# Optimization experiments

Measured on AMD Instinct MI355X. Metric: run time of the kernel, lower is better.

The kernel has to match this reference:

```python
import jax, jax.numpy as jnp
import numpy as np

RRELU_SLOPE = (1.0 / 8.0 + 1.0 / 3.0) / 2.0  # RReLU eval-mode negative slope


def _layer(h, edge_feats, src, dst, W, b, Lw, Lb, n_nodes):
    # per-edge message: concat(src node feat, edge feat) -> linear
    msg = jnp.concatenate([h[src], edge_feats], axis=-1) @ W + b  # [E, H]
    # mean-aggregate messages by destination node (0 for isolated nodes, DGL semantics)
    s = jax.ops.segment_sum(msg, dst, num_segments=n_nodes)  # [N, H]
    cnt = jax.ops.segment_sum(jnp.ones((dst.shape[0], 1), msg.dtype), dst,
                              num_segments=n_nodes)  # [N, 1]
    agg = jnp.where(cnt > 0, s / jnp.maximum(cnt, 1.0), 0.0)
    # self-loop linear add
    agg = agg + h @ Lw + Lb
    # RReLU (eval mode = leaky relu with slope (lower+upper)/2); dropout p=0 is identity
    return jnp.where(agg >= 0, agg, agg * RRELU_SLOPE)


def setup_inputs() -> dict:
    key = jax.random.key(0)
    ks = jax.random.split(key, 12)
    N, E, D, H = 50000, 640000, 128, 128
    sc_in = 1.0 / np.sqrt(2 * D)
    sc_d = 1.0 / np.sqrt(D)
    sc_o = 1.0 / np.sqrt(2 * H)
    return {
        "node_feats": jax.random.normal(ks[0], (N, D), jnp.float32),
        "edge_feats": jax.random.normal(ks[1], (E, D), jnp.float32),
        "src": jax.random.randint(ks[2], (E,), 0, N),
        "dst": jax.random.randint(ks[3], (E,), 0, N),
        "W1": jax.random.uniform(ks[4], (2 * D, H), jnp.float32, -sc_in, sc_in),
        "b1": jnp.zeros((H,), jnp.float32),
        "L1": jax.random.uniform(ks[5], (D, H), jnp.float32, -sc_d, sc_d),
        "lb1": jnp.zeros((H,), jnp.float32),
        "W2": jax.random.uniform(ks[6], (2 * H, H), jnp.float32, -sc_in, sc_in),
        "b2": jnp.zeros((H,), jnp.float32),
        "L2": jax.random.uniform(ks[7], (H, H), jnp.float32, -sc_d, sc_d),
        "lb2": jnp.zeros((H,), jnp.float32),
        "Wo": jax.random.uniform(ks[8], (2 * H, H), jnp.float32, -sc_o, sc_o),
        "bo": jnp.zeros((H,), jnp.float32),
    }


def reference(node_feats, edge_feats, src, dst, W1, b1, L1, lb1, W2, b2, L2, lb2, Wo, bo):
    n = node_feats.shape[0]
    h1 = _layer(node_feats, edge_feats, src, dst, W1, b1, L1, lb1, n)
    h2 = _layer(h1, edge_feats, src, dst, W2, b2, L2, lb2, n)
    multihop = jnp.concatenate([h1, h2], axis=-1)  # [N, 2H]
    return multihop @ Wo + bo
```

## Files before the change

### kernel.cpp

```cpp
#include <hip/hip_runtime.h>
#include <hip/hip_bf16.h>

typedef unsigned short u16;
typedef unsigned int   u32;

using bf16x8 = __attribute__((ext_vector_type(8))) __bf16;
using f32x4  = __attribute__((ext_vector_type(4))) float;

#define SLOPE 0.22916666666666666f
#define CAP 64

static __device__ __forceinline__ u16 f2bf(float f) {
    u32 u = __float_as_uint(f);
    u += 0x7fffu + ((u >> 16) & 1u);
    return (u16)(u >> 16);
}
static __device__ __forceinline__ float bf2f(u16 h) {
    return __uint_as_float(((u32)h) << 16);
}

static __device__ __forceinline__ void gload_lds16(const u16* g, u16* l) {
    __builtin_amdgcn_global_load_lds(
        (const __attribute__((address_space(1))) void*)g,
        (__attribute__((address_space(3))) void*)l,
        16, 0, 0);
}

__global__ void k_prep(const int* __restrict__ src, const int* __restrict__ dst,
                       int* __restrict__ deg, int2* __restrict__ se,
                       const float* __restrict__ node, u16* __restrict__ nfb,
                       const float* __restrict__ W1, const float* __restrict__ L1,
                       const float* __restrict__ W2, const float* __restrict__ L2,
                       const float* __restrict__ Wo, u16* __restrict__ T,
                       int E, int n8, int gE, int gF) {
    int b = blockIdx.x, t = threadIdx.x;
    if (b < gE) {
        int i = b * 256 + t;
        if (i < E) {
            int d = dst[i];
            int p = atomicAdd(&deg[d], 1);
            if (p < CAP) se[(size_t)d * CAP + p] = make_int2(src[i], i);
        }
    } else if (b < gE + gF) {
        int i = (b - gE) * 256 + t;
        if (i < n8) {
            const float4* p = (const float4*)node + (size_t)i * 2;
            float4 a = p[0], c = p[1];
            union { u16 u[8]; uint4 v; } pk;
            pk.u[0] = f2bf(a.x); pk.u[1] = f2bf(a.y); pk.u[2] = f2bf(a.z); pk.u[3] = f2bf(a.w);
            pk.u[4] = f2bf(c.x); pk.u[5] = f2bf(c.y); pk.u[6] = f2bf(c.z); pk.u[7] = f2bf(c.w);
            *((uint4*)nfb + i) = pk.v;
        }
    } else {
        int m = b - gE - gF;
        const float* S; int rowoff;
        switch (m) {
            case 0: S = W1; rowoff = 0;   break;
            case 1: S = W1; rowoff = 128; break;
            case 2: S = L1; rowoff = 0;   break;
            case 3: S = W2; rowoff = 0;   break;
            case 4: S = W2; rowoff = 128; break;
            case 5: S = L2; rowoff = 0;   break;
            case 6: S = Wo; rowoff = 0;   break;
            default: S = Wo; rowoff = 128; break;
        }
        u16* O = T + m * 16384;
        for (int i = t; i < 16384; i += 256) {
            int c = i >> 7, k = i & 127;
            O[i] = f2bf(S[(rowoff + k) * 128 + c]);
        }
    }
}

__global__ void k_aggf(const float* __restrict__ ef, const u16* __restrict__ nfb,
                       const int2* __restrict__ se, const int* __restrict__ deg,
                       u16* __restrict__ EF, u16* __restrict__ A, int N) {
    int w = (blockIdx.x * blockDim.x + threadIdx.x) >> 6;
    int lane = threadIdx.x & 63;
    if (w >= N) return;
    int half = lane >> 5, q = lane & 31;
    int d = deg[w];
    int dc = d < CAP ? d : CAP;
    const int2* sp = se + (size_t)w * CAP;
    float e0 = 0.f, e1 = 0.f, e2 = 0.f, e3 = 0.f;
    float n0 = 0.f, n1 = 0.f, n2 = 0.f, n3 = 0.f;
    int i = 0;
    for (; i + 4 <= dc; i += 4) {
        int2 ia = sp[i + half], ib = sp[i + 2 + half];
        float4 xa = *(const float4*)(ef + (size_t)ia.y * 128 + q * 4);
        uint2  ya = *(const uint2*)(nfb + (size_t)ia.x * 128 + q * 4);
        float4 xb = *(const float4*)(ef + (size_t)ib.y * 128 + q * 4);
        uint2  yb = *(const uint2*)(nfb + (size_t)ib.x * 128 + q * 4);
        e0 += xa.x + xb.x; e1 += xa.y + xb.y; e2 += xa.z + xb.z; e3 += xa.w + xb.w;
        n0 += bf2f((u16)ya.x) + bf2f((u16)yb.x);
        n1 += bf2f((u16)(ya.x >> 16)) + bf2f((u16)(yb.x >> 16));
        n2 += bf2f((u16)ya.y) + bf2f((u16)yb.y);
        n3 += bf2f((u16)(ya.y >> 16)) + bf2f((u16)(yb.y >> 16));
    }
    for (; i + 2 <= dc; i += 2) {
        int2 ia = sp[i + half];
        float4 xa = *(const float4*)(ef + (size_t)ia.y * 128 + q * 4);
        uint2  ya = *(const uint2*)(nfb + (size_t)ia.x * 128 + q * 4);
        e0 += xa.x; e1 += xa.y; e2 += xa.z; e3 += xa.w;
        n0 += bf2f((u16)ya.x); n1 += bf2f((u16)(ya.x >> 16));
        n2 += bf2f((u16)ya.y); n3 += bf2f((u16)(ya.y >> 16));
    }
    if (i + half < dc) {
        int2 ia = sp[i + half];
        float4 xa = *(const float4*)(ef + (size_t)ia.y * 128 + q * 4);
        uint2  ya = *(const uint2*)(nfb + (size_t)ia.x * 128 + q * 4);
        e0 += xa.x; e1 += xa.y; e2 += xa.z; e3 += xa.w;
        n0 += bf2f((u16)ya.x); n1 += bf2f((u16)(ya.x >> 16));
        n2 += bf2f((u16)ya.y); n3 += bf2f((u16)(ya.y >> 16));
    }
    e0 += __shfl_xor(e0, 32); e1 += __shfl_xor(e1, 32);
    e2 += __shfl_xor(e2, 32); e3 += __shfl_xor(e3, 32);
    n0 += __shfl_xor(n0, 32); n1 += __shfl_xor(n1, 32);
    n2 += __shfl_xor(n2, 32); n3 += __shfl_xor(n3, 32);
    float sc = d > 0 ? 1.0f / (float)d : 0.0f;
    union { u16 u[4]; uint2 v; } pk;
    if (half == 0) {
        pk.u[0] = f2bf(e0 * sc); pk.u[1] = f2bf(e1 * sc);
        pk.u[2] = f2bf(e2 * sc); pk.u[3] = f2bf(e3 * sc);
        *(uint2*)(EF + (size_t)w * 128 + q * 4) = pk.v;
    } else {
        pk.u[0] = f2bf(n0 * sc); pk.u[1] = f2bf(n1 * sc);
        pk.u[2] = f2bf(n2 * sc); pk.u[3] = f2bf(n3 * sc);
        *(uint2*)(A + (size_t)w * 128 + q * 4) = pk.v;
    }
}

static __device__ __forceinline__ void add8(float* a, uint4 u) {
    a[0] += bf2f((u16)u.x); a[1] += bf2f((u16)(u.x >> 16));
    a[2] += bf2f((u16)u.y); a[3] += bf2f((u16)(u.y >> 16));
    a[4] += bf2f((u16)u.z); a[5] += bf2f((u16)(u.z >> 16));
    a[6] += bf2f((u16)u.w); a[7] += bf2f((u16)(u.w >> 16));
}

__global__ void k_aggb(const u16* __restrict__ h, const int2* __restrict__ se,
                       const int* __restrict__ deg, u16* __restrict__ out, int N) {
    int w = (blockIdx.x * blockDim.x + threadIdx.x) >> 6;
    int lane = threadIdx.x & 63;
    if (w >= N) return;
    int quarter = lane >> 4, q = lane & 15;
    int d = deg[w];
    int dc = d < CAP ? d : CAP;
    const int2* sp = se + (size_t)w * CAP;
    float a[8] = {0.f, 0.f, 0.f, 0.f, 0.f, 0.f, 0.f, 0.f};
    int i = 0;
    for (; i + 8 <= dc; i += 8) {
        int eA = sp[i + quarter].x, eB = sp[i + 4 + quarter].x;
        uint4 uA = *(const uint4*)(h + (size_t)eA * 128 + q * 8);
        uint4 uB = *(const uint4*)(h + (size_t)eB * 128 + q * 8);
        add8(a, uA); add8(a, uB);
    }
    for (; i + 4 <= dc; i += 4) {
        int eA = sp[i + quarter].x;
        uint4 uA = *(const uint4*)(h + (size_t)eA * 128 + q * 8);
        add8(a, uA);
    }
    if (i + quarter < dc) {
        int eA = sp[i + quarter].x;
        uint4 uA = *(const uint4*)(h + (size_t)eA * 128 + q * 8);
        add8(a, uA);
    }
    #pragma unroll
    for (int j = 0; j < 8; j++) {
        a[j] += __shfl_xor(a[j], 32);
        a[j] += __shfl_xor(a[j], 16);
    }
    if (quarter == 0) {
        float sc = d > 0 ? 1.0f / (float)d : 0.0f;
        union { u16 u[8]; uint4 v; } pk;
        #pragma unroll
        for (int j = 0; j < 8; j++) pk.u[j] = f2bf(a[j] * sc);
        *(uint4*)(out + (size_t)w * 128 + q * 8) = pk.v;
    }
}

#define STAGE_X(LBUF, GPTR)                                                         \
    {                                                                               \
        _Pragma("unroll")                                                           \
        for (int i_ = 0; i_ < 4; i_++) {                                            \
            int id_ = t + i_ * 256;                                                 \
            int r_ = id_ >> 4, c16_ = id_ & 15;                                     \
            int rg_ = row0 + r_; if (rg_ >= N) rg_ = N - 1;                         \
            gload_lds16((GPTR) + (size_t)rg_ * 128 + ((c16_ ^ (r_ & 15)) << 3),     \
                        (LBUF) + id_ * 8);                                          \
        }                                                                           \
    }
#define STAGE_W(GPTR)                                                               \
    {                                                                               \
        _Pragma("unroll")                                                           \
        for (int i_ = 0; i_ < 8; i_++) {                                            \
            int id_ = t + i_ * 256;                                                 \
            int cc_ = id_ >> 4, c16_ = id_ & 15;                                    \
            gload_lds16((GPTR) + cc_ * 128 + ((c16_ ^ (cc_ & 15)) << 3),            \
                        Wl + id_ * 8);                                              \
        }                                                                           \
    }
#define COMPUTE(LBUF)                                                               \
    {                                                                               \
        _Pragma("unroll")                                                           \
        for (int ks_ = 0; ks_ < 4; ks_++) {                                         \
            bf16x8 af_[2], bf_[4];                                                  \
            _Pragma("unroll")                                                       \
            for (int h_ = 0; h_ < 2; h_++) {                                        \
                int r_ = wr * 32 + h_ * 16 + lanelo;                                \
                int ch_ = (ks_ * 4 + lanehi) ^ (r_ & 15);                           \
                af_[h_] = *(const bf16x8*)((LBUF) + r_ * 128 + ch_ * 8);            \
            }                                                                       \
            _Pragma("unroll")                                                       \
            for (int g_ = 0; g_ < 4; g_++) {                                        \
                int cc_ = wc * 64 + g_ * 16 + lanelo;                               \
                int ch_ = (ks_ * 4 + lanehi) ^ (cc_ & 15);                          \
                bf_[g_] = *(const bf16x8*)(Wl + cc_ * 128 + ch_ * 8);               \
            }                                                                       \
            _Pragma("unroll")                                                       \
            for (int h_ = 0; h_ < 2; h_++)                                          \
                _Pragma("unroll")                                                   \
                for (int g_ = 0; g_ < 4; g_++)                                      \
                    acc[h_][g_] = __builtin_amdgcn_mfma_f32_16x16x32_bf16(          \
                        af_[h_], bf_[g_], acc[h_][g_], 0, 0, 0);                    \
        }                                                                           \
    }

__global__ __launch_bounds__(256) void k_gemm1(
    const u16* __restrict__ X0, const u16* __restrict__ X1, const u16* __restrict__ X2,
    const u16* __restrict__ T0, const u16* __restrict__ T1, const u16* __restrict__ T2,
    const float* __restrict__ bm, const int* __restrict__ deg,
    const float* __restrict__ ba, u16* __restrict__ outp, int N) {

    __shared__ u16 Xl[64 * 128];
    __shared__ u16 Wl[128 * 128];

    int t = threadIdx.x, lane = t & 63, wid = t >> 6;
    int lanelo = lane & 15, lanehi = lane >> 4;
    int wr = wid >> 1, wc = wid & 1;
    int row0 = blockIdx.x * 64;

    f32x4 acc[2][4];
    #pragma unroll
    for (int h = 0; h < 2; h++)
        #pragma unroll
        for (int g = 0; g < 4; g++) acc[h][g] = (f32x4){0.f, 0.f, 0.f, 0.f};

    const u16* Xs[3] = {X0, X1, X2};
    const u16* Ts[3] = {T0, T1, T2};
    for (int s = 0; s < 3; s++) {
        __syncthreads();
        STAGE_X(Xl, Xs[s]);
        STAGE_W(Ts[s]);
        __syncthreads();
        COMPUTE(Xl);
    }

    #pragma unroll
    for (int h = 0; h < 2; h++) {
        #pragma unroll
        for (int r = 0; r < 4; r++) {
            int rowt = wr * 32 + h * 16 + lanehi * 4 + r;
            int rg = row0 + rowt;
            if (rg >= N) continue;
            float m = (deg[rg] > 0) ? 1.f : 0.f;
            #pragma unroll
            for (int g = 0; g < 4; g++) {
                int col = wc * 64 + g * 16 + lanelo;
                float v = acc[h][g][r] + ba[col] + m * bm[col];
                v = (v >= 0.f) ? v : v * SLOPE;
                outp[(size_t)rg * 128 + col] = f2bf(v);
            }
        }
    }
}

__global__ __launch_bounds__(256) void k_gemm23(
    const u16* __restrict__ A2, const u16* __restrict__ EF, const u16* __restrict__ H1,
    const u16* __restrict__ TW2a, const u16* __restrict__ TW2b, const u16* __restrict__ TL2,
    const u16* __restrict__ TWoA, const u16* __restrict__ TWoB,
    const float* __restrict__ b2, const float* __restrict__ lb2,
    const float* __restrict__ bo, const int* __restrict__ deg,
    float* __restrict__ outp, int N) {

    __shared__ u16 XA[64 * 128];
    __shared__ u16 XE[64 * 128];
    __shared__ u16 XH[64 * 128];
    __shared__ u16 Wl[128 * 128];

    int t = threadIdx.x, lane = t & 63, wid = t >> 6;
    int lanelo = lane & 15, lanehi = lane >> 4;
    int wr = wid >> 1, wc = wid & 1;
    int row0 = blockIdx.x * 64;

    f32x4 acc[2][4];
    #pragma unroll
    for (int h = 0; h < 2; h++)
        #pragma unroll
        for (int g = 0; g < 4; g++) acc[h][g] = (f32x4){0.f, 0.f, 0.f, 0.f};

    STAGE_X(XA, A2);
    STAGE_X(XE, EF);
    STAGE_X(XH, H1);
    STAGE_W(TW2a);
    __syncthreads();
    COMPUTE(XA);
    __syncthreads();
    STAGE_W(TW2b);
    __syncthreads();
    COMPUTE(XE);
    __syncthreads();
    STAGE_W(TL2);
    __syncthreads();
    COMPUTE(XH);

    #pragma unroll
    for (int h = 0; h < 2; h++) {
        #pragma unroll
        for (int r = 0; r < 4; r++) {
            int rowt = wr * 32 + h * 16 + lanehi * 4 + r;
            int rg = row0 + rowt;
            float m = (rg < N && deg[rg] > 0) ? 1.f : 0.f;
            #pragma unroll
            for (int g = 0; g < 4; g++) {
                int col = wc * 64 + g * 16 + lanelo;
                float v = acc[h][g][r] + lb2[col] + m * b2[col];
                v = (v >= 0.f) ? v : v * SLOPE;
                XA[rowt * 128 + ((((col >> 3) ^ (rowt & 15)) << 3) | (col & 7))] = f2bf(v);
                acc[h][g][r] = 0.f;
            }
        }
    }
    __syncthreads();
    STAGE_W(TWoA);
    __syncthreads();
    COMPUTE(XH);
    __syncthreads();
    STAGE_W(TWoB);
    __syncthreads();
    COMPUTE(XA);

    #pragma unroll
    for (int h = 0; h < 2; h++) {
        #pragma unroll
        for (int r = 0; r < 4; r++) {
            int rowt = wr * 32 + h * 16 + lanehi * 4 + r;
            int rg = row0 + rowt;
            if (rg >= N) continue;
            #pragma unroll
            for (int g = 0; g < 4; g++) {
                int col = wc * 64 + g * 16 + lanelo;
                outp[(size_t)rg * 128 + col] = acc[h][g][r] + bo[col];
            }
        }
    }
}


extern "C" void kernel_launch(void* const* d_in, const int* in_sizes, int n_in,
                              void* d_out, int out_size, void* d_ws, size_t ws_size,
                              hipStream_t stream) {
    const float* node = (const float*)d_in[0];
    const float* ef   = (const float*)d_in[1];
    const int*   src  = (const int*)d_in[2];
    const int*   dst  = (const int*)d_in[3];
    const float* W1   = (const float*)d_in[4];
    const float* b1   = (const float*)d_in[5];
    const float* L1   = (const float*)d_in[6];
    const float* lb1  = (const float*)d_in[7];
    const float* W2   = (const float*)d_in[8];
    const float* b2   = (const float*)d_in[9];
    const float* L2   = (const float*)d_in[10];
    const float* lb2  = (const float*)d_in[11];
    const float* Wo   = (const float*)d_in[12];
    const float* bo   = (const float*)d_in[13];
    int N = in_sizes[0] / 128;
    int E = in_sizes[2];

    char* ws = (char*)d_ws;
    size_t o = 0;
    auto alloc = [&](size_t bytes) {
        void* p = ws + o;
        o = (o + bytes + 511) & ~(size_t)511;
        return p;
    };
    int*  deg = (int*)alloc((size_t)N * 4);
    int2* se  = (int2*)alloc((size_t)N * CAP * 8);
    u16*  T   = (u16*)alloc((size_t)8 * 16384 * 2);
    u16*  nfb = (u16*)alloc((size_t)N * 128 * 2);
    u16*  EF  = (u16*)alloc((size_t)N * 128 * 2);
    u16*  A   = (u16*)alloc((size_t)N * 128 * 2);
    u16*  h1  = (u16*)alloc((size_t)N * 128 * 2);

    hipMemsetAsync(deg, 0, (size_t)N * 4, stream);

    int gE = (E + 255) / 256;
    int n8 = N * 128 / 8;
    int gF = (n8 + 255) / 256;
    k_prep<<<gE + gF + 8, 256, 0, stream>>>(src, dst, deg, se, node, nfb,
                                            W1, L1, W2, L2, Wo, T, E, n8, gE, gF);

    int gA = (N + 3) / 4;
    k_aggf<<<gA, 256, 0, stream>>>(ef, nfb, se, deg, EF, A, N);

    int gb = (N + 63) / 64;
    k_gemm1<<<gb, 256, 0, stream>>>(A, EF, nfb, T, T + 16384, T + 2 * 16384,
                                    b1, deg, lb1, h1, N);
    k_aggb<<<gA, 256, 0, stream>>>(h1, se, deg, A, N);
    k_gemm23<<<gb, 256, 0, stream>>>(A, EF, h1,
                                     T + 3 * 16384, T + 4 * 16384, T + 5 * 16384,
                                     T + 6 * 16384, T + 7 * 16384,
                                     b2, lb2, bo, deg, (float*)d_out, N);
}
```

Before: 211.4 us.

## Fuse neighbor aggregation into layer GEMM kernels, building aggregates directly in LDS

The two standalone aggregation kernels are removed. Their gather-and-mean work now runs inside the GEMM blocks: each wave accumulates 16 destination rows and writes the bf16 means straight into swizzled LDS tiles. The layer-1 kernel still writes the edge-feature mean to global memory for reuse in layer 2. This drops the intermediate A buffer round trip and two launches. In exchange, the latency-bound gathers run in blocks holding about 80KB of LDS, which allows far fewer resident waves than the old lightweight aggregation kernels had to hide memory latency. The mean now divides by the capped degree rather than the true degree.

```diff
diff --git a/kernel.cpp b/kernel.cpp
--- a/kernel.cpp
+++ b/kernel.cpp
@@ -24,6 +24,13 @@
         (const __attribute__((address_space(1))) void*)g,
         (__attribute__((address_space(3))) void*)l,
         16, 0, 0);
+}
+
+static __device__ __forceinline__ void add8(float* a, uint4 u) {
+    a[0] += bf2f((u16)u.x); a[1] += bf2f((u16)(u.x >> 16));
+    a[2] += bf2f((u16)u.y); a[3] += bf2f((u16)(u.y >> 16));
+    a[4] += bf2f((u16)u.z); a[5] += bf2f((u16)(u.z >> 16));
+    a[6] += bf2f((u16)u.w); a[7] += bf2f((u16)(u.w >> 16));
 }
 
 __global__ void k_prep(const int* __restrict__ src, const int* __restrict__ dst,
@@ -69,112 +76,6 @@
             int c = i >> 7, k = i & 127;
             O[i] = f2bf(S[(rowoff + k) * 128 + c]);
         }
-    }
-}
-
-__global__ void k_aggf(const float* __restrict__ ef, const u16* __restrict__ nfb,
-                       const int2* __restrict__ se, const int* __restrict__ deg,
-                       u16* __restrict__ EF, u16* __restrict__ A, int N) {
-    int w = (blockIdx.x * blockDim.x + threadIdx.x) >> 6;
-    int lane = threadIdx.x & 63;
-    if (w >= N) return;
-    int half = lane >> 5, q = lane & 31;
-    int d = deg[w];
-    int dc = d < CAP ? d : CAP;
-    const int2* sp = se + (size_t)w * CAP;
-    float e0 = 0.f, e1 = 0.f, e2 = 0.f, e3 = 0.f;
-    float n0 = 0.f, n1 = 0.f, n2 = 0.f, n3 = 0.f;
-    int i = 0;
-    for (; i + 4 <= dc; i += 4) {
-        int2 ia = sp[i + half], ib = sp[i + 2 + half];
-        float4 xa = *(const float4*)(ef + (size_t)ia.y * 128 + q * 4);
-        uint2  ya = *(const uint2*)(nfb + (size_t)ia.x * 128 + q * 4);
-        float4 xb = *(const float4*)(ef + (size_t)ib.y * 128 + q * 4);
-        uint2  yb = *(const uint2*)(nfb + (size_t)ib.x * 128 + q * 4);
-        e0 += xa.x + xb.x; e1 += xa.y + xb.y; e2 += xa.z + xb.z; e3 += xa.w + xb.w;
-        n0 += bf2f((u16)ya.x) + bf2f((u16)yb.x);
-        n1 += bf2f((u16)(ya.x >> 16)) + bf2f((u16)(yb.x >> 16));
-        n2 += bf2f((u16)ya.y) + bf2f((u16)yb.y);
-        n3 += bf2f((u16)(ya.y >> 16)) + bf2f((u16)(yb.y >> 16));
-    }
-    for (; i + 2 <= dc; i += 2) {
-        int2 ia = sp[i + half];
-        float4 xa = *(const float4*)(ef + (size_t)ia.y * 128 + q * 4);
-        uint2  ya = *(const uint2*)(nfb + (size_t)ia.x * 128 + q * 4);
-        e0 += xa.x; e1 += xa.y; e2 += xa.z; e3 += xa.w;
-        n0 += bf2f((u16)ya.x); n1 += bf2f((u16)(ya.x >> 16));
-        n2 += bf2f((u16)ya.y); n3 += bf2f((u16)(ya.y >> 16));
-    }
-    if (i + half < dc) {
-        int2 ia = sp[i + half];
-        float4 xa = *(const float4*)(ef + (size_t)ia.y * 128 + q * 4);
-        uint2  ya = *(const uint2*)(nfb + (size_t)ia.x * 128 + q * 4);
-        e0 += xa.x; e1 += xa.y; e2 += xa.z; e3 += xa.w;
-        n0 += bf2f((u16)ya.x); n1 += bf2f((u16)(ya.x >> 16));
-        n2 += bf2f((u16)ya.y); n3 += bf2f((u16)(ya.y >> 16));
-    }
-    e0 += __shfl_xor(e0, 32); e1 += __shfl_xor(e1, 32);
-    e2 += __shfl_xor(e2, 32); e3 += __shfl_xor(e3, 32);
-    n0 += __shfl_xor(n0, 32); n1 += __shfl_xor(n1, 32);
-    n2 += __shfl_xor(n2, 32); n3 += __shfl_xor(n3, 32);
-    float sc = d > 0 ? 1.0f / (float)d : 0.0f;
-    union { u16 u[4]; uint2 v; } pk;
-    if (half == 0) {
-        pk.u[0] = f2bf(e0 * sc); pk.u[1] = f2bf(e1 * sc);
-        pk.u[2] = f2bf(e2 * sc); pk.u[3] = f2bf(e3 * sc);
-        *(uint2*)(EF + (size_t)w * 128 + q * 4) = pk.v;
-    } else {
-        pk.u[0] = f2bf(n0 * sc); pk.u[1] = f2bf(n1 * sc);
-        pk.u[2] = f2bf(n2 * sc); pk.u[3] = f2bf(n3 * sc);
-        *(uint2*)(A + (size_t)w * 128 + q * 4) = pk.v;
-    }
-}
-
-static __device__ __forceinline__ void add8(float* a, uint4 u) {
-    a[0] += bf2f((u16)u.x); a[1] += bf2f((u16)(u.x >> 16));
-    a[2] += bf2f((u16)u.y); a[3] += bf2f((u16)(u.y >> 16));
-    a[4] += bf2f((u16)u.z); a[5] += bf2f((u16)(u.z >> 16));
-    a[6] += bf2f((u16)u.w); a[7] += bf2f((u16)(u.w >> 16));
-}
-
-__global__ void k_aggb(const u16* __restrict__ h, const int2* __restrict__ se,
-                       const int* __restrict__ deg, u16* __restrict__ out, int N) {
-    int w = (blockIdx.x * blockDim.x + threadIdx.x) >> 6;
-    int lane = threadIdx.x & 63;
-    if (w >= N) return;
-    int quarter = lane >> 4, q = lane & 15;
-    int d = deg[w];
-    int dc = d < CAP ? d : CAP;
-    const int2* sp = se + (size_t)w * CAP;
-    float a[8] = {0.f, 0.f, 0.f, 0.f, 0.f, 0.f, 0.f, 0.f};
-    int i = 0;
-    for (; i + 8 <= dc; i += 8) {
-        int eA = sp[i + quarter].x, eB = sp[i + 4 + quarter].x;
-        uint4 uA = *(const uint4*)(h + (size_t)eA * 128 + q * 8);
-        uint4 uB = *(const uint4*)(h + (size_t)eB * 128 + q * 8);
-        add8(a, uA); add8(a, uB);
-    }
-    for (; i + 4 <= dc; i += 4) {
-        int eA = sp[i + quarter].x;
-        uint4 uA = *(const uint4*)(h + (size_t)eA * 128 + q * 8);
-        add8(a, uA);
-    }
-    if (i + quarter < dc) {
-        int eA = sp[i + quarter].x;
-        uint4 uA = *(const uint4*)(h + (size_t)eA * 128 + q * 8);
-        add8(a, uA);
-    }
-    #pragma unroll
-    for (int j = 0; j < 8; j++) {
-        a[j] += __shfl_xor(a[j], 32);
-        a[j] += __shfl_xor(a[j], 16);
-    }
-    if (quarter == 0) {
-        float sc = d > 0 ? 1.0f / (float)d : 0.0f;
-        union { u16 u[8]; uint4 v; } pk;
-        #pragma unroll
-        for (int j = 0; j < 8; j++) pk.u[j] = f2bf(a[j] * sc);
-        *(uint4*)(out + (size_t)w * 128 + q * 8) = pk.v;
     }
 }
 
@@ -225,13 +126,16 @@
         }                                                                           \
     }
 
-__global__ __launch_bounds__(256) void k_gemm1(
-    const u16* __restrict__ X0, const u16* __restrict__ X1, const u16* __restrict__ X2,
-    const u16* __restrict__ T0, const u16* __restrict__ T1, const u16* __restrict__ T2,
-    const float* __restrict__ bm, const int* __restrict__ deg,
-    const float* __restrict__ ba, u16* __restrict__ outp, int N) {
-
-    __shared__ u16 Xl[64 * 128];
+__global__ __launch_bounds__(256) void k_g1(
+    const float* __restrict__ ef, const u16* __restrict__ nfb,
+    const int2* __restrict__ se, const int* __restrict__ deg,
+    const u16* __restrict__ TW1a, const u16* __restrict__ TW1b, const u16* __restrict__ TL1,
+    const float* __restrict__ b1, const float* __restrict__ lb1,
+    u16* __restrict__ EFg, u16* __restrict__ h1, int N) {
+
+    __shared__ u16 XA[64 * 128];
+    __shared__ u16 XE[64 * 128];
+    __shared__ u16 XH[64 * 128];
     __shared__ u16 Wl[128 * 128];
 
     int t = threadIdx.x, lane = t & 63, wid = t >> 6;
@@ -245,15 +149,79 @@
         #pragma unroll
         for (int g = 0; g < 4; g++) acc[h][g] = (f32x4){0.f, 0.f, 0.f, 0.f};
 
-    const u16* Xs[3] = {X0, X1, X2};
-    const u16* Ts[3] = {T0, T1, T2};
-    for (int s = 0; s < 3; s++) {
-        __syncthreads();
-        STAGE_X(Xl, Xs[s]);
-        STAGE_W(Ts[s]);
-        __syncthreads();
-        COMPUTE(Xl);
-    }
+    STAGE_X(XH, nfb);
+    STAGE_W(TW1a);
+
+    int t4 = lane >> 4, qq = lane & 15;
+    for (int k = 0; k < 16; k++) {
+        int ln = (k << 2) | wid;
+        int rg = row0 + ln;
+        int d = (rg < N) ? deg[rg] : 0;
+        int dc = d < CAP ? d : CAP;
+        const int2* sp = se + (size_t)rg * CAP;
+        float e[8] = {0.f, 0.f, 0.f, 0.f, 0.f, 0.f, 0.f, 0.f};
+        float n[8] = {0.f, 0.f, 0.f, 0.f, 0.f, 0.f, 0.f, 0.f};
+        int i = 0;
+        for (; i + 8 <= dc; i += 8) {
+            int2 iA = sp[i + t4], iB = sp[i + 4 + t4];
+            const float* ra = ef + (size_t)iA.y * 128 + qq * 8;
+            const float* rb = ef + (size_t)iB.y * 128 + qq * 8;
+            float4 a0 = *(const float4*)ra, a1 = *(const float4*)(ra + 4);
+            float4 c0 = *(const float4*)rb, c1 = *(const float4*)(rb + 4);
+            uint4 ua = *(const uint4*)(nfb + (size_t)iA.x * 128 + qq * 8);
+            uint4 ub = *(const uint4*)(nfb + (size_t)iB.x * 128 + qq * 8);
+            e[0] += a0.x + c0.x; e[1] += a0.y + c0.y; e[2] += a0.z + c0.z; e[3] += a0.w + c0.w;
+            e[4] += a1.x + c1.x; e[5] += a1.y + c1.y; e[6] += a1.z + c1.z; e[7] += a1.w + c1.w;
+            add8(n, ua); add8(n, ub);
+        }
+        for (; i + 4 <= dc; i += 4) {
+            int2 iA = sp[i + t4];
+            const float* ra = ef + (size_t)iA.y * 128 + qq * 8;
+            float4 a0 = *(const float4*)ra, a1 = *(const float4*)(ra + 4);
+            uint4 ua = *(const uint4*)(nfb + (size_t)iA.x * 128 + qq * 8);
+            e[0] += a0.x; e[1] += a0.y; e[2] += a0.z; e[3] += a0.w;
+            e[4] += a1.x; e[5] += a1.y; e[6] += a1.z; e[7] += a1.w;
+            add8(n, ua);
+        }
+        if (i + t4 < dc) {
+            int2 iA = sp[i + t4];
+            const float* ra = ef + (size_t)iA.y * 128 + qq * 8;
+            float4 a0 = *(const float4*)ra, a1 = *(const float4*)(ra + 4);
+            uint4 ua = *(const uint4*)(nfb + (size_t)iA.x * 128 + qq * 8);
+            e[0] += a0.x; e[1] += a0.y; e[2] += a0.z; e[3] += a0.w;
+            e[4] += a1.x; e[5] += a1.y; e[6] += a1.z; e[7] += a1.w;
+            add8(n, ua);
+        }
+        #pragma unroll
+        for (int j = 0; j < 8; j++) {
+            e[j] += __shfl_xor(e[j], 16); e[j] += __shfl_xor(e[j], 32);
+            n[j] += __shfl_xor(n[j], 16); n[j] += __shfl_xor(n[j], 32);
+        }
+        float sc = dc > 0 ? 1.0f / (float)dc : 0.0f;
+        if (t4 == 0) {
+            union { u16 u[8]; uint4 v; } pk;
+            #pragma unroll
+            for (int j = 0; j < 8; j++) pk.u[j] = f2bf(e[j] * sc);
+            *(uint4*)(XE + ln * 128 + ((qq ^ (ln & 15)) << 3)) = pk.v;
+            if (rg < N) *(uint4*)(EFg + (size_t)rg * 128 + qq * 8) = pk.v;
+        } else if (t4 == 1) {
+            union { u16 u[8]; uint4 v; } pk;
+            #pragma unroll
+            for (int j = 0; j < 8; j++) pk.u[j] = f2bf(n[j] * sc);
+            *(uint4*)(XA + ln * 128 + ((qq ^ (ln & 15)) << 3)) = pk.v;
+        }
+    }
+    __syncthreads();
+
+    COMPUTE(XA);
+    __syncthreads();
+    STAGE_W(TW1b);
+    __syncthreads();
+    COMPUTE(XE);
+    __syncthreads();
+    STAGE_W(TL1);
+    __syncthreads();
+    COMPUTE(XH);
 
     #pragma unroll
     for (int h = 0; h < 2; h++) {
@@ -266,21 +234,21 @@
             #pragma unroll
             for (int g = 0; g < 4; g++) {
                 int col = wc * 64 + g * 16 + lanelo;
-                float v = acc[h][g][r] + ba[col] + m * bm[col];
+                float v = acc[h][g][r] + lb1[col] + m * b1[col];
                 v = (v >= 0.f) ? v : v * SLOPE;
-                outp[(size_t)rg * 128 + col] = f2bf(v);
+                h1[(size_t)rg * 128 + col] = f2bf(v);
             }
         }
     }
 }
 
-__global__ __launch_bounds__(256) void k_gemm23(
-    const u16* __restrict__ A2, const u16* __restrict__ EF, const u16* __restrict__ H1,
+__global__ __launch_bounds__(256) void k_g23(
+    const u16* __restrict__ EFg, const u16* __restrict__ H1,
+    const int2* __restrict__ se, const int* __restrict__ deg,
     const u16* __restrict__ TW2a, const u16* __restrict__ TW2b, const u16* __restrict__ TL2,
     const u16* __restrict__ TWoA, const u16* __restrict__ TWoB,
     const float* __restrict__ b2, const float* __restrict__ lb2,
-    const float* __restrict__ bo, const int* __restrict__ deg,
-    float* __restrict__ outp, int N) {
+    const float* __restrict__ bo, float* __restrict__ outp, int N) {
 
     __shared__ u16 XA[64 * 128];
     __shared__ u16 XE[64 * 128];
@@ -298,11 +266,49 @@
         #pragma unroll
         for (int g = 0; g < 4; g++) acc[h][g] = (f32x4){0.f, 0.f, 0.f, 0.f};
 
-    STAGE_X(XA, A2);
-    STAGE_X(XE, EF);
+    STAGE_X(XE, EFg);
     STAGE_X(XH, H1);
     STAGE_W(TW2a);
-    __syncthreads();
+
+    int t4 = lane >> 4, qq = lane & 15;
+    for (int k = 0; k < 16; k++) {
+        int ln = (k << 2) | wid;
+        int rg = row0 + ln;
+        int d = (rg < N) ? deg[rg] : 0;
+        int dc = d < CAP ? d : CAP;
+        const int2* sp = se + (size_t)rg * CAP;
+        float n[8] = {0.f, 0.f, 0.f, 0.f, 0.f, 0.f, 0.f, 0.f};
+        int i = 0;
+        for (; i + 8 <= dc; i += 8) {
+            int eA = sp[i + t4].x, eB = sp[i + 4 + t4].x;
+            uint4 ua = *(const uint4*)(H1 + (size_t)eA * 128 + qq * 8);
+            uint4 ub = *(const uint4*)(H1 + (size_t)eB * 128 + qq * 8);
+            add8(n, ua); add8(n, ub);
+        }
+        for (; i + 4 <= dc; i += 4) {
+            int eA = sp[i + t4].x;
+            uint4 ua = *(const uint4*)(H1 + (size_t)eA * 128 + qq * 8);
+            add8(n, ua);
+        }
+        if (i + t4 < dc) {
+            int eA = sp[i + t4].x;
+            uint4 ua = *(const uint4*)(H1 + (size_t)eA * 128 + qq * 8);
+            add8(n, ua);
+        }
+        #pragma unroll
+        for (int j = 0; j < 8; j++) {
+            n[j] += __shfl_xor(n[j], 16); n[j] += __shfl_xor(n[j], 32);
+        }
+        if (t4 == 0) {
+            float sc = dc > 0 ? 1.0f / (float)dc : 0.0f;
+            union { u16 u[8]; uint4 v; } pk;
+            #pragma unroll
+            for (int j = 0; j < 8; j++) pk.u[j] = f2bf(n[j] * sc);
+            *(uint4*)(XA + ln * 128 + ((qq ^ (ln & 15)) << 3)) = pk.v;
+        }
+    }
+    __syncthreads();
+
     COMPUTE(XA);
     __syncthreads();
     STAGE_W(TW2b);
@@ -388,7 +394,6 @@
     u16*  T   = (u16*)alloc((size_t)8 * 16384 * 2);
     u16*  nfb = (u16*)alloc((size_t)N * 128 * 2);
     u16*  EF  = (u16*)alloc((size_t)N * 128 * 2);
-    u16*  A   = (u16*)alloc((size_t)N * 128 * 2);
     u16*  h1  = (u16*)alloc((size_t)N * 128 * 2);
 
     hipMemsetAsync(deg, 0, (size_t)N * 4, stream);
@@ -399,15 +404,11 @@
     k_prep<<<gE + gF + 8, 256, 0, stream>>>(src, dst, deg, se, node, nfb,
                                             W1, L1, W2, L2, Wo, T, E, n8, gE, gF);
 
-    int gA = (N + 3) / 4;
-    k_aggf<<<gA, 256, 0, stream>>>(ef, nfb, se, deg, EF, A, N);
-
     int gb = (N + 63) / 64;
-    k_gemm1<<<gb, 256, 0, stream>>>(A, EF, nfb, T, T + 16384, T + 2 * 16384,
-                                    b1, deg, lb1, h1, N);
-    k_aggb<<<gA, 256, 0, stream>>>(h1, se, deg, A, N);
-    k_gemm23<<<gb, 256, 0, stream>>>(A, EF, h1,
-                                     T + 3 * 16384, T + 4 * 16384, T + 5 * 16384,
-                                     T + 6 * 16384, T + 7 * 16384,
-                                     b2, lb2, bo, deg, (float*)d_out, N);
-}
+    k_g1<<<gb, 256, 0, stream>>>(ef, nfb, se, deg, T, T + 16384, T + 2 * 16384,
+                                 b1, lb1, EF, h1, N);
+    k_g23<<<gb, 256, 0, stream>>>(EF, h1, se, deg,
+                                  T + 3 * 16384, T + 4 * 16384, T + 5 * 16384,
+                                  T + 6 * 16384, T + 7 * 16384,
+                                  b2, lb2, bo, (float*)d_out, N);
+}
```

Result: slower. 302.4 us (+43.0%).
